# Kernel optimization log

Hardware: AMD Instinct MI355X
Metric: run time of the kernel (lower is better)

Reference implementation:

```python
import jax, jax.numpy as jnp
import numpy as np

B, S, V, I, NB = 256, 512, 30000, 100, 19
H4 = 4 * I
BOS, EOS = 17, 18


def setup_inputs() -> dict:
    key = jax.random.key(0)
    ks = jax.random.split(key, 18)
    u = lambda k, shp, s: jax.random.uniform(k, shp, jnp.float32, -s, s)
    sc = 1.0 / np.sqrt(I)
    sc1 = 1.0 / np.sqrt(2 * I)
    sc2 = 1.0 / np.sqrt(100)
    trans = u(ks[17], (NB, NB), 0.1)
    trans = trans.at[:, BOS].set(-10000.0).at[EOS, :].set(-10000.0)
    return {
        "x": jax.random.randint(ks[0], (B, S, 1), 0, V),
        "target": jax.random.randint(ks[1], (B, S), 0, 17),
        "emb": jax.random.normal(ks[2], (V, I), jnp.float32),
        "Wih_f": u(ks[3], (H4, I), sc), "Whh_f": u(ks[4], (H4, I), sc),
        "bih_f": u(ks[5], (H4,), sc), "bhh_f": u(ks[6], (H4,), sc),
        "Wih_b": u(ks[7], (H4, I), sc), "Whh_b": u(ks[8], (H4, I), sc),
        "bih_b": u(ks[9], (H4,), sc), "bhh_b": u(ks[10], (H4,), sc),
        "W1": u(ks[11], (100, 2 * I), sc1), "b1": u(ks[12], (100,), sc1),
        "W2": u(ks[13], (NB, 100), sc2), "b2": u(ks[14], (NB,), sc2),
        "transitions": trans,
    }


def _lstm(xs, Wih, Whh, bih, bhh):
    # xs: [B,S,I]; PyTorch gate order i,f,g,o; h0=c0=0
    pre = jnp.einsum('bsi,gi->bsg', xs, Wih) + bih + bhh  # [B,S,4H]
    H = Whh.shape[1]
    b = xs.shape[0]
    def step(carry, p):
        h, c = carry
        g = p + h @ Whh.T
        i, f, gg, o = jnp.split(g, 4, axis=-1)
        c = jax.nn.sigmoid(f) * c + jax.nn.sigmoid(i) * jnp.tanh(gg)
        h = jax.nn.sigmoid(o) * jnp.tanh(c)
        return (h, c), h
    h0 = jnp.zeros((b, H), xs.dtype)
    _, hs = jax.lax.scan(step, (h0, h0), jnp.swapaxes(pre, 0, 1))
    return jnp.swapaxes(hs, 0, 1)  # [B,S,H]


def _crf_nll(em, tags, T):
    # em: [B,S,NB] emissions; tags: [B,S]; T: [NB,NB] transitions
    # gold path score (mask is all-ones)
    e_sc = jnp.take_along_axis(em, tags[..., None], axis=2).squeeze(-1).sum(1)
    t_sc = T[tags[:, :-1], tags[:, 1:]].sum(1) + T[BOS, tags[:, 0]] + T[tags[:, -1], EOS]
    scores = e_sc + t_sc
    # log-partition via forward recurrence
    alphas = T[BOS][None, :] + em[:, 0]  # [B,NB]
    def step(a, e_t):
        # a: [B,NB] prev; broadcast to [B, prev_tag, cur_tag]
        return jax.nn.logsumexp(a[:, :, None] + T[None] + e_t[:, None, :], axis=1), None
    alphas, _ = jax.lax.scan(step, alphas, jnp.swapaxes(em[:, 1:], 0, 1))
    partition = jax.nn.logsumexp(alphas + T[:, EOS][None, :], axis=1)
    return -jnp.mean(scores - partition)


def reference(x, target, emb, Wih_f, Whh_f, bih_f, bhh_f, Wih_b, Whh_b, bih_b, bhh_b, W1, b1, W2, b2, transitions):
    xe = emb[x[:, :, 0]]  # [B,S,I]
    hf = _lstm(xe, Wih_f, Whh_f, bih_f, bhh_f)
    hb = _lstm(xe[:, ::-1], Wih_b, Whh_b, bih_b, bhh_b)[:, ::-1]
    h = jnp.concatenate([hf, hb], axis=-1)  # [B,S,2I]
    em = (h @ W1.T + b1) @ W2.T + b2  # [B,S,NB]
    return _crf_nll(em, target, transitions)
```

## Files before the change

### kernel.cpp

```cpp
#include <hip/hip_runtime.h>
#include <hip/hip_bf16.h>

#define DI __device__ __forceinline__

constexpr int B_ = 256, S_ = 512, I_ = 100, NB_ = 19, H4_ = 400;
constexpr int BOS_ = 17, EOS_ = 18;
constexpr int BS_ = B_ * S_;
constexpr int V_ = 30000;

typedef float v2f __attribute__((ext_vector_type(2)));
typedef float v4f __attribute__((ext_vector_type(4)));

DI float sigf(float x) { return 1.0f / (1.0f + __expf(-x)); }
DI float tanhf_(float x) {
  float e = __expf(-2.0f * fabsf(x));
  float r = (1.0f - e) / (1.0f + e);
  return copysignf(r, x);
}

DI float qred(float a) {
  a += __int_as_float(__builtin_amdgcn_mov_dpp(__float_as_int(a), 0xB1, 0xF, 0xF, true));
  a += __int_as_float(__builtin_amdgcn_mov_dpp(__float_as_int(a), 0x4E, 0xF, 0xF, true));
  return a;
}

__global__ __launch_bounds__(256) void prep_kernel(
    const float* __restrict__ W1, const float* __restrict__ b1,
    const float* __restrict__ W2, const float* __restrict__ b2,
    const float* __restrict__ bih_f, const float* __restrict__ bhh_f,
    const float* __restrict__ bih_b, const float* __restrict__ bhh_b,
    float* __restrict__ M2, float* __restrict__ c0, float* __restrict__ biasAll) {
  int t = threadIdx.x;
  for (int c = t; c < 800; c += 256)
    biasAll[c] = (c < 400) ? (bih_f[c] + bhh_f[c]) : (bih_b[c - 400] + bhh_b[c - 400]);
  if (t < 19) {
    float acc = b2[t];
    for (int j = 0; j < 100; ++j) acc += W2[t * 100 + j] * b1[j];
    c0[t] = acc;
  }
  for (int i = t; i < 19 * 200; i += 256) {
    int v = i / 200, d = i - v * 200;
    float acc = 0.f;
    for (int j = 0; j < 100; ++j) acc += W2[v * 100 + j] * W1[j * 200 + d];
    M2[i] = acc;
  }
  for (int i = 3800 + t; i < 4000; i += 256) M2[i] = 0.f;
}

__global__ __launch_bounds__(256) void ewbuild_kernel(
    const float* __restrict__ emb, const float* __restrict__ Wih_f,
    const float* __restrict__ Wih_b, const float* __restrict__ biasAll,
    float* __restrict__ EW) {
  __shared__ __align__(16) float Al[64 * 100];
  __shared__ __align__(16) float Bl[80 * 100];
  int tid = threadIdx.x;
  int ct = blockIdx.x;
  int rt = blockIdx.y;
  int row0 = rt * 64;
  const float* Wsrc = (ct < 5) ? (Wih_f + (size_t)ct * 8000)
                               : (Wih_b + (size_t)(ct - 5) * 8000);
  const float4* bsrc = (const float4*)Wsrc;
  float4* bdst = (float4*)Bl;
  for (int i = tid; i < 2000; i += 256) bdst[i] = bsrc[i];
  float4* adst = (float4*)Al;
  for (int i = tid; i < 1600; i += 256) {
    int r = i / 25, qq = i - r * 25;
    int v = min(row0 + r, V_ - 1);
    adst[i] = ((const float4*)(emb + (size_t)v * 100))[qq];
  }
  __syncthreads();

  int tr = tid >> 4, tc = tid & 15;
  int r0 = tr * 4, c0l = tc * 5;
  float acc[4][5];
#pragma unroll
  for (int i = 0; i < 4; ++i)
#pragma unroll
    for (int j = 0; j < 5; ++j) acc[i][j] = 0.f;

  for (int k = 0; k < 100; k += 4) {
    float4 a[4], b[5];
#pragma unroll
    for (int i = 0; i < 4; ++i) a[i] = *(const float4*)&Al[(r0 + i) * 100 + k];
#pragma unroll
    for (int j = 0; j < 5; ++j) b[j] = *(const float4*)&Bl[(c0l + j) * 100 + k];
#pragma unroll
    for (int i = 0; i < 4; ++i)
#pragma unroll
      for (int j = 0; j < 5; ++j) {
        acc[i][j] += a[i].x * b[j].x;
        acc[i][j] += a[i].y * b[j].y;
        acc[i][j] += a[i].z * b[j].z;
        acc[i][j] += a[i].w * b[j].w;
      }
  }

  int colb = (ct < 5) ? (ct * 80 + c0l) : (400 + (ct - 5) * 80 + c0l);
#pragma unroll
  for (int i = 0; i < 4; ++i) {
    int vr = row0 + r0 + i;
    if (vr < V_) {
#pragma unroll
      for (int j = 0; j < 5; ++j)
        EW[(size_t)vr * 800 + colb + j] = acc[i][j] + biasAll[ct * 80 + c0l + j];
    }
  }
}

__global__ __launch_bounds__(400, 1) void scan_fused2_kernel(
    const int* __restrict__ x, const float* __restrict__ EW,
    const float* __restrict__ Whh_f, const float* __restrict__ Whh_b,
    float* __restrict__ hf, float* __restrict__ hb) {
  __shared__ __align__(16) float h_q[2][2][4][28];
  int bid = blockIdx.x;
  int pair = bid >> 1, dir = bid & 1;
  int tid = threadIdx.x;
  int u = tid >> 2, q = tid & 3;
  const float* Whh = dir ? Whh_b : Whh_f;
  float* hdir = dir ? hb : hf;
  float* houtA = hdir + (size_t)(pair * 2) * 51200;
  float* houtB = hdir + (size_t)(pair * 2 + 1) * 51200;
  const int* xbA = x + (size_t)(pair * 2) * 512;
  const int* xbB = x + (size_t)(pair * 2 + 1) * 512;
  const int dirb = dir * 400;
  const int s0 = dir ? 511 : 0, sstep = dir ? -1 : 1;

  v2f w2[4][13];
#pragma unroll
  for (int g = 0; g < 4; ++g) {
    const float* pr = Whh + (size_t)(g * 100 + u) * 100 + q * 25;
#pragma unroll
    for (int k = 0; k < 12; ++k) w2[g][k] = v2f{pr[2 * k], pr[2 * k + 1]};
    w2[g][12] = v2f{pr[24], 0.f};
  }
  const int uq = u / 25, up = u - uq * 25;
  float* houtme = (q & 1) ? houtB : houtA;

  for (int i = tid; i < 448; i += 400) ((float*)h_q)[i] = 0.f;

  float pc[4] = {0.f, 0.f, 0.f, 0.f}, pn[4];
  int xnA = xbA[s0 + sstep], xnB = xbB[s0 + sstep];
  {
    int xcA = xbA[s0], xcB = xbB[s0];
    if (q < 2) {
      const float* ewr = EW + (size_t)(q ? xcB : xcA) * 800 + dirb + u;
#pragma unroll
      for (int g = 0; g < 4; ++g) pc[g] = ewr[g * 100];
    }
  }
  float c = 0.f;
  __syncthreads();

  for (int t = 0; t < 512; ++t) {
    int s = s0 + sstep * t;
    pn[0] = pn[1] = pn[2] = pn[3] = 0.f;
    if (q < 2) {
      const float* ewr = EW + (size_t)(q ? xnB : xnA) * 800 + dirb + u;
#pragma unroll
      for (int g = 0; g < 4; ++g) pn[g] = ewr[g * 100];
    }
    int s2 = min(511, max(0, s + 2 * sstep));
    xnA = xbA[s2]; xnB = xbB[s2];

    int cb = t & 1, nb = cb ^ 1;
    const float* hA = &h_q[cb][0][q][0];
    const float* hB = &h_q[cb][1][q][0];
    v2f ra[4], rb[4];
#pragma unroll
    for (int g = 0; g < 4; ++g) { ra[g] = v2f{0.f, 0.f}; rb[g] = v2f{0.f, 0.f}; }
#pragma unroll
    for (int m = 0; m < 6; ++m) {
      v4f a4 = *(const v4f*)(hA + 4 * m);
      v4f b4 = *(const v4f*)(hB + 4 * m);
      v2f alo = v2f{a4.x, a4.y}, ahi = v2f{a4.z, a4.w};
      v2f blo = v2f{b4.x, b4.y}, bhi = v2f{b4.z, b4.w};
#pragma unroll
      for (int g = 0; g < 4; ++g) {
        ra[g] += w2[g][2 * m] * alo;
        ra[g] += w2[g][2 * m + 1] * ahi;
        rb[g] += w2[g][2 * m] * blo;
        rb[g] += w2[g][2 * m + 1] * bhi;
      }
    }
    {
      v2f at = *(const v2f*)(hA + 24);
      v2f bt = *(const v2f*)(hB + 24);
#pragma unroll
      for (int g = 0; g < 4; ++g) { ra[g] += w2[g][12] * at; rb[g] += w2[g][12] * bt; }
    }

    float gate[4];
#pragma unroll
    for (int g = 0; g < 4; ++g) {
      float sa = qred(ra[g].x + ra[g].y);
      float sb = qred(rb[g].x + rb[g].y);
      gate[g] = ((q & 1) ? sb : sa) + pc[g];
    }
    c = sigf(gate[1]) * c + sigf(gate[0]) * tanhf_(gate[2]);
    float h = sigf(gate[3]) * tanhf_(c);
    if (q < 2) {
      h_q[nb][q][uq][up] = h;
      houtme[(size_t)s * 100 + u] = h;
    }
    pc[0] = pn[0]; pc[1] = pn[1]; pc[2] = pn[2]; pc[3] = pn[3];
    __syncthreads();
  }
}

__global__ __launch_bounds__(128) void emis_kernel(
    const float* __restrict__ hfB, const float* __restrict__ hbB,
    const float* __restrict__ M2g, const float* __restrict__ c0g,
    float* __restrict__ em) {
  __shared__ __align__(16) float hrow[32 * 204];
  __shared__ __align__(16) float M2l[4000];
  __shared__ float c0l[20];
  int tid = threadIdx.x;
  int row0 = blockIdx.x * 32;
  for (int i = tid; i < 800; i += 128) {
    int r = i / 25, q = i - r * 25;
    *(float4*)&hrow[r * 204 + q * 4] =
        *(const float4*)(hfB + (size_t)(row0 + r) * 100 + q * 4);
    *(float4*)&hrow[r * 204 + 100 + q * 4] =
        *(const float4*)(hbB + (size_t)(row0 + r) * 100 + q * 4);
  }
  for (int i = tid; i < 1000; i += 128) ((float4*)M2l)[i] = ((const float4*)M2g)[i];
  if (tid < 20) c0l[tid] = (tid < 19) ? c0g[tid] : 0.f;
  __syncthreads();

  int r = tid >> 2, q = tid & 3;
  int v0 = q * 5;
  float acc[5] = {0.f, 0.f, 0.f, 0.f, 0.f};
  for (int k = 0; k < 200; k += 4) {
    float4 h4 = *(const float4*)&hrow[r * 204 + k];
#pragma unroll
    for (int i = 0; i < 5; ++i) {
      float4 m4 = *(const float4*)&M2l[(v0 + i) * 200 + k];
      acc[i] += h4.x * m4.x + h4.y * m4.y + h4.z * m4.z + h4.w * m4.w;
    }
  }
  int nv = (q == 3) ? 4 : 5;
  for (int i = 0; i < nv; ++i)
    em[(size_t)(row0 + r) * 19 + v0 + i] = acc[i] + c0l[v0 + i];
}

__global__ __launch_bounds__(64) void crf_kernel(
    const float* __restrict__ em, const int* __restrict__ target,
    const float* __restrict__ T, float* __restrict__ res) {
  __shared__ float em_l[512 * 19];
  __shared__ float T_l[361];
  __shared__ int tgt_l[512];
  constexpr float LOG2E = 1.4426950408889634f;
  constexpr float LN2 = 0.6931471805599453f;
  int b = blockIdx.x, lane = threadIdx.x;
  const float* emsrc = em + (size_t)b * 512 * 19;
  for (int i = lane; i < 512 * 19; i += 64) em_l[i] = emsrc[i] * LOG2E;
  for (int i = lane; i < 361; i += 64) T_l[i] = T[i] * LOG2E;
  for (int i = lane; i < 512; i += 64) tgt_l[i] = target[b * 512 + i];
  __syncthreads();

  float sc = 0.f;
  for (int t = lane; t < 512; t += 64) {
    int tg = tgt_l[t];
    sc += em_l[t * 19 + tg];
    if (t < 511) sc += T_l[tg * 19 + tgt_l[t + 1]];
  }
#pragma unroll
  for (int off = 32; off >= 1; off >>= 1) sc += __shfl_xor(sc, off);

  int v = (lane < 17) ? lane : 0;
  float Tcol[17];
#pragma unroll
  for (int u = 0; u < 17; ++u) Tcol[u] = T_l[u * 19 + v];
  float a[17];
#pragma unroll
  for (int u = 0; u < 17; ++u) a[u] = T_l[BOS_ * 19 + u] + em_l[u];

  for (int t = 1; t < 512; ++t) {
    float xx[17];
#pragma unroll
    for (int u = 0; u < 17; ++u) xx[u] = a[u] + Tcol[u];
    float m = xx[0];
#pragma unroll
    for (int u = 1; u < 17; ++u) m = fmaxf(m, xx[u]);
    float s0 = 0.f, s1 = 0.f, s2 = 0.f, s3 = 0.f;
#pragma unroll
    for (int u = 0; u < 16; u += 4) {
      s0 += exp2f(xx[u] - m);
      s1 += exp2f(xx[u + 1] - m);
      s2 += exp2f(xx[u + 2] - m);
      s3 += exp2f(xx[u + 3] - m);
    }
    s0 += exp2f(xx[16] - m);
    float na = m + log2f((s0 + s1) + (s2 + s3)) + em_l[t * 19 + v];
#pragma unroll
    for (int u = 0; u < 17; ++u) a[u] = __shfl(na, u, 64);
  }

  float xx[17];
#pragma unroll
  for (int u = 0; u < 17; ++u) xx[u] = a[u] + T_l[u * 19 + EOS_];
  float m = xx[0];
#pragma unroll
  for (int u = 1; u < 17; ++u) m = fmaxf(m, xx[u]);
  float ssum = 0.f;
#pragma unroll
  for (int u = 0; u < 17; ++u) ssum += exp2f(xx[u] - m);
  float part = m + log2f(ssum);

  if (lane == 0) {
    float score = sc + T_l[BOS_ * 19 + tgt_l[0]] + T_l[tgt_l[511] * 19 + EOS_];
    res[b] = (score - part) * LN2;
  }
}

__global__ void final_kernel(const float* __restrict__ res, float* __restrict__ out) {
  int lane = threadIdx.x;
  float s = 0.f;
  for (int i = lane; i < 256; i += 64) s += res[i];
#pragma unroll
  for (int off = 32; off >= 1; off >>= 1) s += __shfl_xor(s, off);
  if (lane == 0) out[0] = -s * (1.0f / 256.0f);
}

extern "C" void kernel_launch(void* const* d_in, const int* in_sizes, int n_in,
                              void* d_out, int out_size, void* d_ws, size_t ws_size,
                              hipStream_t stream) {
  const int*   x      = (const int*)d_in[0];
  const int*   target = (const int*)d_in[1];
  const float* emb    = (const float*)d_in[2];
  const float* Wih_f  = (const float*)d_in[3];
  const float* Whh_f  = (const float*)d_in[4];
  const float* bih_f  = (const float*)d_in[5];
  const float* bhh_f  = (const float*)d_in[6];
  const float* Wih_b  = (const float*)d_in[7];
  const float* Whh_b  = (const float*)d_in[8];
  const float* bih_b  = (const float*)d_in[9];
  const float* bhh_b  = (const float*)d_in[10];
  const float* W1     = (const float*)d_in[11];
  const float* b1     = (const float*)d_in[12];
  const float* W2     = (const float*)d_in[13];
  const float* b2     = (const float*)d_in[14];
  const float* trans  = (const float*)d_in[15];
  float* out = (float*)d_out;

  float* ws = (float*)d_ws;
  float* em      = ws;
  float* M2      = em + (size_t)BS_ * 19;
  float* c0      = M2 + 4000;
  float* biasAll = c0 + 64;
  float* res     = biasAll + 1024;
  float* hfbuf   = res + 256;
  float* hbbuf   = hfbuf + (size_t)BS_ * 100;
  float* EW      = hbbuf + (size_t)BS_ * 100;

  prep_kernel<<<1, 256, 0, stream>>>(W1, b1, W2, b2, bih_f, bhh_f, bih_b, bhh_b,
                                     M2, c0, biasAll);
  ewbuild_kernel<<<dim3(10, (V_ + 63) / 64), 256, 0, stream>>>(emb, Wih_f, Wih_b,
                                                               biasAll, EW);
  scan_fused2_kernel<<<256, 400, 0, stream>>>(x, EW, Whh_f, Whh_b, hfbuf, hbbuf);
  emis_kernel<<<BS_ / 32, 128, 0, stream>>>(hfbuf, hbbuf, M2, c0, em);
  crf_kernel<<<B_, 64, 0, stream>>>(em, target, trans, res);
  final_kernel<<<1, 64, 0, stream>>>(res, out);
}
```

Baseline: 1.354 ms.

## Stage token ids in LDS, spread gate-input loads across quads, restride EW tile

The scan kernel now copies the token ids for both sequences into shared memory once. Each lane loads one gate pre-activation instead of lanes 0-1 each loading four, and that value is added before the quad DPP reduction, so it reaches every lane for free. The per-step load is prefetched two steps ahead with a manually unrolled two-step loop, and the cell update is limited to lanes q<2. The ewbuild GEMM switches to interleaved row and column assignment (stride 16) so that stores and LDS reads are coalesced, and launch bounds are relaxed to allow two blocks per CU. These changes add an extra branch in the serial step and raise shared-memory use.

```diff
diff --git a/kernel.cpp b/kernel.cpp
--- a/kernel.cpp
+++ b/kernel.cpp
@@ -71,7 +71,6 @@
   __syncthreads();
 
   int tr = tid >> 4, tc = tid & 15;
-  int r0 = tr * 4, c0l = tc * 5;
   float acc[4][5];
 #pragma unroll
   for (int i = 0; i < 4; ++i)
@@ -81,9 +80,9 @@
   for (int k = 0; k < 100; k += 4) {
     float4 a[4], b[5];
 #pragma unroll
-    for (int i = 0; i < 4; ++i) a[i] = *(const float4*)&Al[(r0 + i) * 100 + k];
-#pragma unroll
-    for (int j = 0; j < 5; ++j) b[j] = *(const float4*)&Bl[(c0l + j) * 100 + k];
+    for (int i = 0; i < 4; ++i) a[i] = *(const float4*)&Al[(tr + 16 * i) * 100 + k];
+#pragma unroll
+    for (int j = 0; j < 5; ++j) b[j] = *(const float4*)&Bl[(tc + 16 * j) * 100 + k];
 #pragma unroll
     for (int i = 0; i < 4; ++i)
 #pragma unroll
@@ -95,23 +94,26 @@
       }
   }
 
-  int colb = (ct < 5) ? (ct * 80 + c0l) : (400 + (ct - 5) * 80 + c0l);
+  int base = (ct < 5) ? (ct * 80) : (400 + (ct - 5) * 80);
 #pragma unroll
   for (int i = 0; i < 4; ++i) {
-    int vr = row0 + r0 + i;
+    int vr = row0 + tr + 16 * i;
     if (vr < V_) {
 #pragma unroll
-      for (int j = 0; j < 5; ++j)
-        EW[(size_t)vr * 800 + colb + j] = acc[i][j] + biasAll[ct * 80 + c0l + j];
-    }
-  }
-}
-
-__global__ __launch_bounds__(400, 1) void scan_fused2_kernel(
+      for (int j = 0; j < 5; ++j) {
+        int cc = tc + 16 * j;
+        EW[(size_t)vr * 800 + base + cc] = acc[i][j] + biasAll[ct * 80 + cc];
+      }
+    }
+  }
+}
+
+__global__ __launch_bounds__(400, 2) void scan_fused3_kernel(
     const int* __restrict__ x, const float* __restrict__ EW,
     const float* __restrict__ Whh_f, const float* __restrict__ Whh_b,
     float* __restrict__ hf, float* __restrict__ hb) {
   __shared__ __align__(16) float h_q[2][2][4][28];
+  __shared__ int xl[2][512];
   int bid = blockIdx.x;
   int pair = bid >> 1, dir = bid & 1;
   int tid = threadIdx.x;
@@ -125,6 +127,11 @@
   const int dirb = dir * 400;
   const int s0 = dir ? 511 : 0, sstep = dir ? -1 : 1;
 
+  for (int i = tid; i < 512; i += 400) {
+    xl[0][i] = xbA[s0 + sstep * i];
+    xl[1][i] = xbB[s0 + sstep * i];
+  }
+
   v2f w2[4][13];
 #pragma unroll
   for (int g = 0; g < 4; ++g) {
@@ -134,34 +141,20 @@
     w2[g][12] = v2f{pr[24], 0.f};
   }
   const int uq = u / 25, up = u - uq * 25;
-  float* houtme = (q & 1) ? houtB : houtA;
+  float* houtme = (q == 1) ? houtB : houtA;
 
   for (int i = tid; i < 448; i += 400) ((float*)h_q)[i] = 0.f;
-
-  float pc[4] = {0.f, 0.f, 0.f, 0.f}, pn[4];
-  int xnA = xbA[s0 + sstep], xnB = xbB[s0 + sstep];
-  {
-    int xcA = xbA[s0], xcB = xbB[s0];
-    if (q < 2) {
-      const float* ewr = EW + (size_t)(q ? xcB : xcA) * 800 + dirb + u;
-#pragma unroll
-      for (int g = 0; g < 4; ++g) pc[g] = ewr[g * 100];
-    }
-  }
   float c = 0.f;
   __syncthreads();
 
-  for (int t = 0; t < 512; ++t) {
+  const float* ewq = EW + dirb + q * 100 + u;
+  float pA0 = ewq[(size_t)xl[0][0] * 800];
+  float pB0 = ewq[(size_t)xl[1][0] * 800];
+  float pA1 = ewq[(size_t)xl[0][1] * 800];
+  float pB1 = ewq[(size_t)xl[1][1] * 800];
+
+  auto STEP = [&](int t, float& pA, float& pB) {
     int s = s0 + sstep * t;
-    pn[0] = pn[1] = pn[2] = pn[3] = 0.f;
-    if (q < 2) {
-      const float* ewr = EW + (size_t)(q ? xnB : xnA) * 800 + dirb + u;
-#pragma unroll
-      for (int g = 0; g < 4; ++g) pn[g] = ewr[g * 100];
-    }
-    int s2 = min(511, max(0, s + 2 * sstep));
-    xnA = xbA[s2]; xnB = xbB[s2];
-
     int cb = t & 1, nb = cb ^ 1;
     const float* hA = &h_q[cb][0][q][0];
     const float* hB = &h_q[cb][1][q][0];
@@ -192,18 +185,27 @@
     float gate[4];
 #pragma unroll
     for (int g = 0; g < 4; ++g) {
-      float sa = qred(ra[g].x + ra[g].y);
-      float sb = qred(rb[g].x + rb[g].y);
-      gate[g] = ((q & 1) ? sb : sa) + pc[g];
-    }
-    c = sigf(gate[1]) * c + sigf(gate[0]) * tanhf_(gate[2]);
-    float h = sigf(gate[3]) * tanhf_(c);
+      float sa = ra[g].x + ra[g].y + ((q == g) ? pA : 0.0f);
+      float sb = rb[g].x + rb[g].y + ((q == g) ? pB : 0.0f);
+      float qa = qred(sa);
+      float qb = qred(sb);
+      gate[g] = (q & 1) ? qb : qa;
+    }
     if (q < 2) {
+      c = sigf(gate[1]) * c + sigf(gate[0]) * tanhf_(gate[2]);
+      float h = sigf(gate[3]) * tanhf_(c);
       h_q[nb][q][uq][up] = h;
       houtme[(size_t)s * 100 + u] = h;
     }
-    pc[0] = pn[0]; pc[1] = pn[1]; pc[2] = pn[2]; pc[3] = pn[3];
+    int i2 = min(t + 2, 511);
+    pA = ewq[(size_t)xl[0][i2] * 800];
+    pB = ewq[(size_t)xl[1][i2] * 800];
     __syncthreads();
+  };
+
+  for (int t = 0; t < 512; t += 2) {
+    STEP(t, pA0, pB0);
+    STEP(t + 1, pA1, pB1);
   }
 }
 
@@ -357,7 +359,7 @@
                                      M2, c0, biasAll);
   ewbuild_kernel<<<dim3(10, (V_ + 63) / 64), 256, 0, stream>>>(emb, Wih_f, Wih_b,
                                                                biasAll, EW);
-  scan_fused2_kernel<<<256, 400, 0, stream>>>(x, EW, Whh_f, Whh_b, hfbuf, hbbuf);
+  scan_fused3_kernel<<<256, 400, 0, stream>>>(x, EW, Whh_f, Whh_b, hfbuf, hbbuf);
   emis_kernel<<<BS_ / 32, 128, 0, stream>>>(hfbuf, hbbuf, M2, c0, em);
   crf_kernel<<<B_, 64, 0, stream>>>(em, target, trans, res);
   final_kernel<<<1, 64, 0, stream>>>(res, out);
```

New measurement: 1.230 ms. -9.2%, faster.
